# Performance work log

Hardware: AMD Instinct MI355X
Metric: run time of the kernel (lower is better)

Reference implementation:

```python
import jax, jax.numpy as jnp
import numpy as np

HEADS = 16
DIM_HEAD = 64
DIM = 1024
SEQ = 2048
BATCH = 1
THR_MIN = 0.01
THR_MAX = 0.9
LN_EPS = 1e-5
NEG = -jnp.finfo(jnp.float32).max


def _ln(x, gamma):
    # torch F.layer_norm over last dim, beta fixed to zeros
    mu = jnp.mean(x, axis=-1, keepdims=True)
    var = jnp.mean(jnp.square(x - mu), axis=-1, keepdims=True)
    return (x - mu) * jax.lax.rsqrt(var + LN_EPS) * gamma


def setup_inputs() -> dict:
    key = jax.random.key(0)
    ks = jax.random.split(key, 8)
    s = 0.02  # realistic init scale for weights
    return {
        "x": jax.random.normal(ks[0], (BATCH, SEQ, DIM), jnp.float32),
        "gamma_norm": jnp.ones((DIM,), jnp.float32),
        "Wq": jax.random.normal(ks[1], (DIM, HEADS * DIM_HEAD), jnp.float32) * s,
        "Wk": jax.random.normal(ks[2], (DIM, HEADS * DIM_HEAD), jnp.float32) * s,
        "Wv": jax.random.normal(ks[3], (DIM, HEADS * DIM_HEAD), jnp.float32) * s,
        "Wout": jax.random.normal(ks[4], (HEADS * DIM_HEAD, DIM), jnp.float32) * s,
        "gamma_out": jnp.ones((DIM,), jnp.float32),
        "W_gcn0": jax.random.normal(ks[5], (DIM_HEAD, DIM_HEAD), jnp.float32) * s,
        "b_gcn0": jnp.zeros((DIM_HEAD,), jnp.float32),
        "W_gcn1": jax.random.normal(ks[6], (DIM_HEAD, DIM_HEAD), jnp.float32) * s,
        "b_gcn1": jnp.zeros((DIM_HEAD,), jnp.float32),
        "W_lin": jax.random.normal(ks[7], (DIM_HEAD, DIM_HEAD), jnp.float32) * s,
        "b_lin": jnp.zeros((DIM_HEAD,), jnp.float32),
    }


def reference(x, gamma_norm, Wq, Wk, Wv, Wout, gamma_out,
              W_gcn0, b_gcn0, W_gcn1, b_gcn1, W_lin, b_lin):
    b, n, _ = x.shape
    h, d = HEADS, DIM_HEAD
    scale = d ** -0.5

    xn = _ln(x, gamma_norm)
    # projections, split heads: b n (h d) -> b h n d
    q = (xn @ Wq).reshape(b, n, h, d).transpose(0, 2, 1, 3) * scale
    k = (xn @ Wk).reshape(b, n, h, d).transpose(0, 2, 1, 3)
    v = (xn @ Wv).reshape(b, n, h, d).transpose(0, 2, 1, 3)

    sim = jnp.einsum("bhid,bhjd->bhij", q, k)
    causal_mask = jnp.triu(jnp.ones((n, n), bool), 1)
    sim = jnp.where(causal_mask, NEG, sim)
    attn = jax.nn.softmax(sim.astype(jnp.float32), axis=-1)  # [b,h,n,n]

    out = jnp.einsum("bhij,bhjd->bhid", attn, v)

    # --- attention-derived adjacency GCN path ---
    adj = attn.reshape(b * h, n, n) + jnp.eye(n, dtype=attn.dtype)
    adj = jnp.clip(adj, 0.0, 1.0)
    adj = jnp.where(adj < THR_MIN, 0.0, adj)
    adj = jnp.where(adj > THR_MAX, 1.0, adj)

    g = v.reshape(b * h, n, d)
    deg = jnp.sum(adj, axis=-1, keepdims=True)  # [bh, n, 1]
    # GCN layer 0 (skip connection, exact GELU like nn.GELU())
    g = jax.nn.gelu(jnp.matmul(adj, g @ W_gcn0 + b_gcn0) / deg + g, approximate=False)
    # GCN layer 1
    g = jax.nn.gelu(jnp.matmul(adj, g @ W_gcn1 + b_gcn1) / deg + g, approximate=False)
    # final linear (dropout inactive in eval)
    g = g @ W_lin + b_lin

    out = out + g.reshape(b, h, n, d)

    # merge heads: b h n d -> b n (h d), output projection + LayerNorm
    out = out.transpose(0, 2, 1, 3).reshape(b, n, h * d)
    out = _ln(out @ Wout, gamma_out)
    return out
```

## Files before the change

kernel.cpp:

```cpp
#include <hip/hip_runtime.h>
#include <hip/hip_bf16.h>
#include <math.h>
#include <stdint.h>

#define DEV __device__ __forceinline__

typedef unsigned short u16;
typedef __attribute__((ext_vector_type(8))) short s16x8;
typedef __attribute__((ext_vector_type(4))) float f32x4;
typedef __attribute__((ext_vector_type(16))) float f32x16;
typedef __attribute__((ext_vector_type(4))) unsigned u32x4;

static constexpr int SEQ = 2048;
static constexpr int DIM = 1024;
static constexpr int HEADS = 16;
static constexpr int QKVLD = 3072;
static constexpr int TOT32 = 2080;

DEV u16 f2bf(float f) {
  unsigned u = __float_as_uint(f);
  u = u + 0x7FFFu + ((u >> 16) & 1u);
  return (u16)(u >> 16);
}
DEV float bf2f(u16 b) { return __uint_as_float(((unsigned)b) << 16); }
DEV float gelu_exact(float x) { return 0.5f * x * (1.0f + erff(x * 0.70710678118654752f)); }

DEV unsigned pkbf(float lo, float hi) {
  __hip_bfloat162 h = __float22bfloat162_rn(make_float2(lo, hi));
  unsigned r; __builtin_memcpy(&r, &h, 4); return r;
}

#define MFMA16(a, b, c) __builtin_amdgcn_mfma_f32_16x16x32_bf16(a, b, c, 0, 0, 0)
#define MFMA32(a, b, c) __builtin_amdgcn_mfma_f32_32x32x16_bf16(a, b, c, 0, 0, 0)

DEV s16x8 u4_to_s8(u32x4 u) { union { u32x4 a; s16x8 b; } c; c.a = u; return c.b; }

DEV void build_frags(const float* p, int hi, s16x8* fr) {
  unsigned pw[4][2];
#pragma unroll
  for (int rq = 0; rq < 4; ++rq) {
    pw[rq][0] = pkbf(p[4 * rq + 0], p[4 * rq + 1]);
    pw[rq][1] = pkbf(p[4 * rq + 2], p[4 * rq + 3]);
  }
#pragma unroll
  for (int m = 0; m < 2; ++m) {
    unsigned x0 = __shfl_xor(pw[2 * m + 1][0], 32);
    unsigned x1 = __shfl_xor(pw[2 * m + 1][1], 32);
    unsigned y0 = __shfl_xor(pw[2 * m][0], 32);
    unsigned y1 = __shfl_xor(pw[2 * m][1], 32);
    u32x4 u;
    u[0] = hi ? x0 : pw[2 * m][0];
    u[1] = hi ? x1 : pw[2 * m][1];
    u[2] = hi ? pw[2 * m + 1][0] : y0;
    u[3] = hi ? pw[2 * m + 1][1] : y1;
    fr[m] = u4_to_s8(u);
  }
}

template<bool OUT_BF16>
__global__ __launch_bounds__(256) void ln_rows(const float* __restrict__ in,
                                               const float* __restrict__ gamma,
                                               void* __restrict__ outp) {
  int row = blockIdx.x;
  const float* x = in + (size_t)row * DIM;
  float v[4];
  float s = 0.f;
#pragma unroll
  for (int e = 0; e < 4; ++e) { v[e] = x[threadIdx.x + 256 * e]; s += v[e]; }
  __shared__ float red[8];
  int lane = threadIdx.x & 63, wid = threadIdx.x >> 6;
#pragma unroll
  for (int off = 32; off; off >>= 1) s += __shfl_xor(s, off);
  if (lane == 0) red[wid] = s;
  __syncthreads();
  float mean = (red[0] + red[1] + red[2] + red[3]) * (1.0f / DIM);
  float vs = 0.f;
#pragma unroll
  for (int e = 0; e < 4; ++e) { float d = v[e] - mean; vs += d * d; }
#pragma unroll
  for (int off = 32; off; off >>= 1) vs += __shfl_xor(vs, off);
  __syncthreads();
  if (lane == 0) red[wid] = vs;
  __syncthreads();
  float var = (red[0] + red[1] + red[2] + red[3]) * (1.0f / DIM);
  float rstd = rsqrtf(var + 1e-5f);
#pragma unroll
  for (int e = 0; e < 4; ++e) {
    int c = threadIdx.x + 256 * e;
    float o = (v[e] - mean) * rstd * gamma[c];
    if (OUT_BF16) ((u16*)outp)[(size_t)row * DIM + c] = f2bf(o);
    else          ((float*)outp)[(size_t)row * DIM + c] = o;
  }
}

__global__ __launch_bounds__(256) void wt_all(
    const float* __restrict__ Wq, const float* __restrict__ Wk, const float* __restrict__ Wv,
    const float* __restrict__ Wout, const float* __restrict__ Wg0,
    const float* __restrict__ Wg1, const float* __restrict__ Wlin,
    u16* __restrict__ WqkvT, u16* __restrict__ WoT,
    u16* __restrict__ Wg0T, u16* __restrict__ Wg1T, u16* __restrict__ WlinT) {
  int z = blockIdx.z;
  const float* src; u16* dst; int R, C, c0, r0;
  if (z < 4) {
    src = (z == 0) ? Wq : (z == 1) ? Wk : (z == 2) ? Wv : Wout;
    dst = (z == 0) ? WqkvT : (z == 1) ? WqkvT + (size_t)DIM * DIM
        : (z == 2) ? WqkvT + (size_t)2 * DIM * DIM : WoT;
    R = DIM; C = DIM; c0 = blockIdx.x * 64; r0 = blockIdx.y * 64;
  } else {
    if (blockIdx.x >= 3 || blockIdx.y > 0) return;
    src = (blockIdx.x == 0) ? Wg0 : (blockIdx.x == 1) ? Wg1 : Wlin;
    dst = (blockIdx.x == 0) ? Wg0T : (blockIdx.x == 1) ? Wg1T : WlinT;
    R = 64; C = 64; c0 = 0; r0 = 0;
  }
  __shared__ float tile[64][65];
  int tx = threadIdx.x & 63, ty = threadIdx.x >> 6;
  for (int rr = ty; rr < 64; rr += 4)
    tile[rr][tx] = src[(size_t)(r0 + rr) * C + c0 + tx];
  __syncthreads();
  for (int rr = ty; rr < 64; rr += 4)
    dst[(size_t)(c0 + rr) * R + r0 + tx] = f2bf(tile[tx][rr]);
}

__global__ __launch_bounds__(256) void pack_qkv(const u16* __restrict__ QKV,
                                                u16* __restrict__ Kp, u16* __restrict__ Vp) {
  int bx = blockIdx.x, h = blockIdx.y;
  int tid = threadIdx.x, wid = tid >> 6, lane = tid & 63;
  int l31 = lane & 31, hi = lane >> 5;
  if (bx < 64) {
    int jb = bx, fi = wid;
    s16x8 v = *(const s16x8*)(QKV + (size_t)(jb * 32 + l31) * QKVLD + 1024 + h * 64 + fi * 16 + hi * 8);
    *(s16x8*)(Kp + ((size_t)(h * 64 + jb) * 4 + fi) * 512 + lane * 8) = v;
  } else {
    int jb16 = bx - 64;
    __shared__ u16 t[16][72];
    if (tid < 128) {
      int r = tid >> 3, c = (tid & 7) * 8;
      *(s16x8*)&t[r][c] = *(const s16x8*)(QKV + (size_t)(jb16 * 16 + r) * QKVLD + 2048 + h * 64 + c);
    }
    __syncthreads();
    if (wid < 2) {
      int dh = wid;
      s16x8 v;
#pragma unroll
      for (int e = 0; e < 8; ++e) v[e] = (short)t[hi * 8 + e][dh * 32 + l31];
      *(s16x8*)(Vp + ((size_t)(h * 128 + jb16) * 2 + dh) * 512 + lane * 8) = v;
    }
  }
}

__global__ __launch_bounds__(256) void gemm_pack(
    const u16* __restrict__ Asrc, int ld, const u16* __restrict__ Wt,
    const float* __restrict__ bias, u16* __restrict__ Hp) {
  int bx = blockIdx.x, h = blockIdx.y;
  __shared__ __align__(16) u16 Ws[64][72];
  __shared__ __align__(16) u16 tt[64][72];
  int tid = threadIdx.x, lane = tid & 63, wid = tid >> 6;
  int l15 = lane & 15, lhi = lane >> 4;
  {
    int r = tid >> 2, cc = (tid & 3) * 8;
    *(s16x8*)&Ws[r][cc] = *(const s16x8*)(Wt + r * 64 + cc);
    *(s16x8*)&Ws[r][cc + 32] = *(const s16x8*)(Wt + r * 64 + cc + 32);
  }
  __syncthreads();
  int j = bx * 64 + wid * 16 + l15;
  const u16* arow = Asrc + (size_t)j * ld + h * 64;
  s16x8 a0 = *(const s16x8*)(arow + lhi * 8);
  s16x8 a1 = *(const s16x8*)(arow + 32 + lhi * 8);
  f32x4 acc[4];
#pragma unroll
  for (int c = 0; c < 4; ++c) {
    acc[c] = f32x4{0.f, 0.f, 0.f, 0.f};
    s16x8 b0 = *(const s16x8*)&Ws[c * 16 + l15][lhi * 8];
    s16x8 b1 = *(const s16x8*)&Ws[c * 16 + l15][32 + lhi * 8];
    acc[c] = MFMA16(a0, b0, acc[c]);
    acc[c] = MFMA16(a1, b1, acc[c]);
  }
  int rl = wid * 16 + lhi * 4;
#pragma unroll
  for (int c = 0; c < 4; ++c)
#pragma unroll
    for (int r = 0; r < 4; ++r)
      tt[rl + r][c * 16 + l15] = f2bf(acc[c][r] + bias[c * 16 + l15]);
  __syncthreads();
  int l31 = lane & 31, hi = lane >> 5;
#pragma unroll
  for (int dh = 0; dh < 2; ++dh) {
    s16x8 v;
#pragma unroll
    for (int e = 0; e < 8; ++e) v[e] = (short)tt[wid * 16 + hi * 8 + e][dh * 32 + l31];
    *(s16x8*)(Hp + ((size_t)(h * 128 + bx * 4 + wid) * 2 + dh) * 512 + lane * 8) = v;
  }
}

DEV void gload_lds16(const u16* g, u16* l) {
  __builtin_amdgcn_global_load_lds(
      (const __attribute__((address_space(1))) unsigned int*)g,
      (__attribute__((address_space(3))) unsigned int*)(unsigned int)(uintptr_t)l,
      16, 0, 0);
}
template<int BM, int BN, bool OUT_F32>
__global__ __launch_bounds__(256) void gemm_t(const u16* __restrict__ A,
                                              const u16* __restrict__ Bt,
                                              void* __restrict__ Cout,
                                              int Nn, int K, int Nq, float qs) {
  constexpr int MI = BM / 32;
  constexpr int NI = BN / 32;
  __shared__ __align__(16) u16 As[BM][64];
  __shared__ __align__(16) u16 Bs[BN][64];
  int tid = threadIdx.x, lane = tid & 63, wid = tid >> 6;
  int l15 = lane & 15, lhi = lane >> 4;
  int nwg = gridDim.x * gridDim.y;
  int flat = blockIdx.y * gridDim.x + blockIdx.x;
  int q8 = nwg >> 3, r8 = nwg & 7;
  int xcd = flat & 7, idx = flat >> 3;
  int wg = (xcd < r8) ? xcd * (q8 + 1) + idx : r8 * (q8 + 1) + (xcd - r8) * q8 + idx;
  int bx = wg % gridDim.x, by = wg / gridDim.x;
  int n0 = bx * BN, m0 = by * BM;
  int wr = wid >> 1, wc = wid & 1;
  float scale = (n0 < Nq) ? qs : 1.0f;
  f32x4 acc[MI][NI];
#pragma unroll
  for (int mi = 0; mi < MI; ++mi)
#pragma unroll
    for (int ni = 0; ni < NI; ++ni) acc[mi][ni] = f32x4{0.f, 0.f, 0.f, 0.f};
  int srow = lane >> 3;
  int scol = ((lane & 7) ^ srow) * 8;
  for (int k0 = 0; k0 < K; k0 += 64) {
    __syncthreads();
#pragma unroll
    for (int i = 0; i < BM / 32; ++i) {
      int row0 = (wid * (BM / 32) + i) * 8;
      gload_lds16(A + (size_t)(m0 + row0 + srow) * K + k0 + scol, &As[row0][0]);
    }
#pragma unroll
    for (int i = 0; i < BN / 32; ++i) {
      int row0 = (wid * (BN / 32) + i) * 8;
      gload_lds16(Bt + (size_t)(n0 + row0 + srow) * K + k0 + scol, &Bs[row0][0]);
    }
    __syncthreads();
#pragma unroll
    for (int ks = 0; ks < 2; ++ks) {
      s16x8 af[MI], bf[NI];
#pragma unroll
      for (int mi = 0; mi < MI; ++mi) {
        int row = wr * (BM / 2) + mi * 16 + l15;
        int c8 = (ks * 4 + lhi) ^ (row & 7);
        af[mi] = *(const s16x8*)&As[row][c8 * 8];
      }
#pragma unroll
      for (int ni = 0; ni < NI; ++ni) {
        int row = wc * (BN / 2) + ni * 16 + l15;
        int c8 = (ks * 4 + lhi) ^ (row & 7);
        bf[ni] = *(const s16x8*)&Bs[row][c8 * 8];
      }
#pragma unroll
      for (int mi = 0; mi < MI; ++mi)
#pragma unroll
        for (int ni = 0; ni < NI; ++ni)
          acc[mi][ni] = MFMA16(af[mi], bf[ni], acc[mi][ni]);
    }
  }
  int orow0 = m0 + wr * (BM / 2), ocol0 = n0 + wc * (BN / 2);
#pragma unroll
  for (int mi = 0; mi < MI; ++mi)
#pragma unroll
    for (int ni = 0; ni < NI; ++ni)
#pragma unroll
      for (int r = 0; r < 4; ++r) {
        int row = orow0 + mi * 16 + lhi * 4 + r;
        int col = ocol0 + ni * 16 + l15;
        float vv = acc[mi][ni][r] * scale;
        if (OUT_F32) ((float*)Cout)[(size_t)row * Nn + col] = vv;
        else         ((u16*)Cout)[(size_t)row * Nn + col] = f2bf(vv);
      }
}

__global__ __launch_bounds__(256) void small_gemm_add(
    const u16* __restrict__ A, int ldo, const u16* __restrict__ Wt,
    const float* __restrict__ bias, const float* __restrict__ addsrc,
    u16* __restrict__ outp) {
  __shared__ __align__(16) u16 Ws[64][72];
  int tid = threadIdx.x, lane = tid & 63, wid = tid >> 6;
  int l15 = lane & 15, lhi = lane >> 4;
  int m0 = blockIdx.x * 64;
  {
    int r = tid >> 2, cc = (tid & 3) * 8;
    *(s16x8*)&Ws[r][cc] = *(const s16x8*)(Wt + r * 64 + cc);
    *(s16x8*)&Ws[r][cc + 32] = *(const s16x8*)(Wt + r * 64 + cc + 32);
  }
  __syncthreads();
  int R = m0 + wid * 16 + l15;
  const u16* arow = A + (size_t)(R >> 4) * ldo + (R & 15) * 64;
  s16x8 a0 = *(const s16x8*)(arow + lhi * 8);
  s16x8 a1 = *(const s16x8*)(arow + 32 + lhi * 8);
  f32x4 acc[4];
#pragma unroll
  for (int c = 0; c < 4; ++c) {
    acc[c] = f32x4{0.f, 0.f, 0.f, 0.f};
    s16x8 b0 = *(const s16x8*)&Ws[c * 16 + l15][lhi * 8];
    s16x8 b1 = *(const s16x8*)&Ws[c * 16 + l15][32 + lhi * 8];
    acc[c] = MFMA16(a0, b0, acc[c]);
    acc[c] = MFMA16(a1, b1, acc[c]);
  }
  int orow = m0 + wid * 16 + lhi * 4;
#pragma unroll
  for (int c = 0; c < 4; ++c)
#pragma unroll
    for (int r = 0; r < 4; ++r) {
      int col = c * 16 + l15;
      size_t idx = (size_t)(orow + r) * 64 + col;
      outp[idx] = f2bf(acc[c][r] + bias[col] + addsrc[idx]);
    }
}

static constexpr float NEGB = -3.0e38f;
DEV int crowf(int r, int hi) { return (r & 3) + 8 * (r >> 2) + 4 * hi; }

template<bool STORE_ADJ>
__global__ __launch_bounds__(512, 4) void attn_pv(
    const u16* __restrict__ QKV, const u16* __restrict__ Kp, const u16* __restrict__ Vp,
    float* __restrict__ mbuf, float* __restrict__ lbuf, float* __restrict__ degb,
    float* __restrict__ oatt, u16* __restrict__ adjS, unsigned char* __restrict__ maskb) {
  int tid = threadIdx.x, wq = tid >> 6, lane = tid & 63;
  int l31 = lane & 31, hi = lane >> 5;
  int h = blockIdx.x & 15, sidx = blockIdx.x >> 4;
  int s = 63 - sidx;

  __shared__ float cmb[4][2][16][64];
  __shared__ float smf[8][32], slf[8][32], sdg[8][32];

  int qbase = s * 32;
  int cums = (s * (s + 1)) >> 1;
  int n = s + 1;
  int c_lo = (n * wq) >> 3, c_hi = (n * (wq + 1)) >> 3;

  s16x8 qf[4];
#pragma unroll
  for (int fi = 0; fi < 4; ++fi)
    qf[fi] = *(const s16x8*)(QKV + (size_t)(qbase + l31) * QKVLD + h * 64 + fi * 16 + hi * 8);

  float mp = NEGB, lp = 0.f;
  for (int jb = c_lo; jb < c_hi; ++jb) {
    f32x16 sa;
#pragma unroll
    for (int r = 0; r < 16; ++r) sa[r] = 0.f;
#pragma unroll
    for (int fi = 0; fi < 4; ++fi) {
      s16x8 kf = *(const s16x8*)(Kp + ((size_t)(h * 64 + jb) * 4 + fi) * 512 + lane * 8);
      sa = MFMA32(kf, qf[fi], sa);
    }
    bool diag = (jb == s);
    float vmax = NEGB;
#pragma unroll
    for (int r = 0; r < 16; ++r) {
      float v = sa[r];
      if (diag && (crowf(r, hi) > l31)) v = NEGB;
      sa[r] = v; vmax = fmaxf(vmax, v);
    }
    float mn = fmaxf(mp, vmax);
    float es = 0.f;
#pragma unroll
    for (int r = 0; r < 16; ++r) es += __expf(sa[r] - mn);
    lp = lp * __expf(mp - mn) + es;
    mp = mn;
  }
  {
    float mo = __shfl_xor(mp, 32), lo = __shfl_xor(lp, 32);
    float mn = fmaxf(mp, mo);
    lp = lp * __expf(mp - mn) + lo * __expf(mo - mn);
    mp = mn;
  }
  if (hi == 0) { smf[wq][l31] = mp; slf[wq][l31] = lp; }
  __syncthreads();
  float mt = NEGB, lt = 0.f;
#pragma unroll
  for (int w2 = 0; w2 < 8; ++w2) {
    float mo = smf[w2][l31], lo = slf[w2][l31];
    float mn = fmaxf(mt, mo);
    lt = lt * __expf(mt - mn) + lo * __expf(mo - mn);
    mt = mn;
  }
  float invl = 1.0f / lt;
  if (wq == 0 && hi == 0) {
    mbuf[(size_t)h * SEQ + qbase + l31] = mt;
    lbuf[(size_t)h * SEQ + qbase + l31] = lt;
  }

  f32x16 pv0, pv1;
#pragma unroll
  for (int r = 0; r < 16; ++r) { pv0[r] = 0.f; pv1[r] = 0.f; }
  float dacc = 0.f;
  for (int jb = c_lo; jb < c_hi; ++jb) {
    f32x16 sa;
#pragma unroll
    for (int r = 0; r < 16; ++r) sa[r] = 0.f;
#pragma unroll
    for (int fi = 0; fi < 4; ++fi) {
      s16x8 kf = *(const s16x8*)(Kp + ((size_t)(h * 64 + jb) * 4 + fi) * 512 + lane * 8);
      sa = MFMA32(kf, qf[fi], sa);
    }
    bool diag = (jb == s);
    float p[16];
#pragma unroll
    for (int r = 0; r < 16; ++r) {
      bool valid = !diag || (crowf(r, hi) <= l31);
      p[r] = valid ? __expf(sa[r] - mt) * invl : 0.f;
    }
    s16x8 pf[2]; build_frags(p, hi, pf);
#pragma unroll
    for (int m = 0; m < 2; ++m) {
      const u16* vb = Vp + ((size_t)(h * 128 + jb * 2 + m) * 2) * 512;
      pv0 = MFMA32(pf[m], *(const s16x8*)(vb + lane * 8), pv0);
      pv1 = MFMA32(pf[m], *(const s16x8*)(vb + 512 + lane * 8), pv1);
    }
    float as0 = 0.f, as1 = 0.f;
#pragma unroll
    for (int r = 0; r < 16; ++r) {
      float pp = p[r];
      float a = (diag && (crowf(r, hi) == l31)) ? 1.f
                : ((pp < 0.01f) ? 0.f : ((pp > 0.9f) ? 1.f : pp));
      p[r] = a; dacc += a;
      if (r < 8) as0 += a; else as1 += a;
    }
    unsigned flags = (__ballot(as0 > 0.f) ? 1u : 0u) | (__ballot(as1 > 0.f) ? 2u : 0u);
    if (STORE_ADJ && flags) {
      s16x8 af[2]; build_frags(p, hi, af);
      size_t fb = ((size_t)h * TOT32 + cums + jb) * 2;
#pragma unroll
      for (int m = 0; m < 2; ++m) if ((flags >> m) & 1u)
        *(s16x8*)(adjS + (fb + m) * 512 + lane * 8) = af[m];
    }
    if (lane == 0) maskb[(size_t)h * TOT32 + cums + jb] = (unsigned char)flags;
  }
  dacc += __shfl_xor(dacc, 32);
  if (hi == 0) sdg[wq][l31] = dacc;
  if (wq >= 4) {
#pragma unroll
    for (int r = 0; r < 16; ++r) {
      cmb[wq - 4][0][r][lane] = pv0[r];
      cmb[wq - 4][1][r][lane] = pv1[r];
    }
  }
  __syncthreads();
  if (wq < 4) {
#pragma unroll
    for (int r = 0; r < 16; ++r) {
      pv0[r] += cmb[wq][0][r][lane];
      pv1[r] += cmb[wq][1][r][lane];
    }
  }
  __syncthreads();
  if (wq == 2 || wq == 3) {
#pragma unroll
    for (int r = 0; r < 16; ++r) {
      cmb[wq - 2][0][r][lane] = pv0[r];
      cmb[wq - 2][1][r][lane] = pv1[r];
    }
  }
  __syncthreads();
  if (wq < 2) {
#pragma unroll
    for (int r = 0; r < 16; ++r) {
      pv0[r] += cmb[wq][0][r][lane];
      pv1[r] += cmb[wq][1][r][lane];
    }
  }
  __syncthreads();
  if (wq == 1) {
#pragma unroll
    for (int r = 0; r < 16; ++r) {
      cmb[0][0][r][lane] = pv0[r];
      cmb[0][1][r][lane] = pv1[r];
    }
  }
  __syncthreads();
  if (wq == 0) {
    if (hi == 0) {
      float dt = 0.f;
#pragma unroll
      for (int w2 = 0; w2 < 8; ++w2) dt += sdg[w2][l31];
      degb[(size_t)h * SEQ + qbase + l31] = dt;
    }
#pragma unroll
    for (int r = 0; r < 16; ++r) {
      pv0[r] += cmb[0][0][r][lane];
      pv1[r] += cmb[0][1][r][lane];
    }
#pragma unroll
    for (int r = 0; r < 16; ++r) {
      int qr = qbase + crowf(r, hi);
      oatt[(size_t)qr * DIM + h * 64 + l31] = pv0[r];
      oatt[(size_t)qr * DIM + h * 64 + 32 + l31] = pv1[r];
    }
  }
}

template<bool READ_ADJ>
__global__ __launch_bounds__(512, 4) void gcn_apply(
    const u16* __restrict__ QKV, const u16* __restrict__ Kp,
    const u16* __restrict__ Hp, const u16* __restrict__ adjS,
    const unsigned char* __restrict__ maskb,
    const float* __restrict__ mbuf, const float* __restrict__ lbuf,
    const float* __restrict__ degb,
    const u16* __restrict__ skip, int skipld, u16* __restrict__ outp) {
  int tid = threadIdx.x, wq = tid >> 6, lane = tid & 63;
  int l31 = lane & 31, hi = lane >> 5;
  int h = blockIdx.x & 15, sidx = blockIdx.x >> 4;
  int s = 63 - sidx;

  __shared__ float cmb[4][2][16][64];

  int qbase = s * 32;
  int cums = (s * (s + 1)) >> 1;
  int n = s + 1;
  int c_lo = (n * wq) >> 3, c_hi = (n * (wq + 1)) >> 3;

  f32x16 gc0, gc1;
#pragma unroll
  for (int r = 0; r < 16; ++r) { gc0[r] = 0.f; gc1[r] = 0.f; }

  if constexpr (READ_ADJ) {
    for (int jb = c_lo; jb < c_hi; ++jb) {
      unsigned flags = maskb[(size_t)h * TOT32 + cums + jb];
      if (!flags) continue;
      size_t fb = ((size_t)h * TOT32 + cums + jb) * 2;
#pragma unroll
      for (int m = 0; m < 2; ++m) if ((flags >> m) & 1u) {
        s16x8 af = *(const s16x8*)(adjS + (fb + m) * 512 + lane * 8);
        const u16* hb = Hp + ((size_t)(h * 128 + jb * 2 + m) * 2) * 512;
        gc0 = MFMA32(af, *(const s16x8*)(hb + lane * 8), gc0);
        gc1 = MFMA32(af, *(const s16x8*)(hb + 512 + lane * 8), gc1);
      }
    }
  } else {
    s16x8 qf[4];
#pragma unroll
    for (int fi = 0; fi < 4; ++fi)
      qf[fi] = *(const s16x8*)(QKV + (size_t)(qbase + l31) * QKVLD + h * 64 + fi * 16 + hi * 8);
    float mt = mbuf[(size_t)h * SEQ + qbase + l31];
    float invl = 1.0f / lbuf[(size_t)h * SEQ + qbase + l31];
    for (int jb = c_lo; jb < c_hi; ++jb) {
      unsigned flags = maskb[(size_t)h * TOT32 + cums + jb];
      if (!flags) continue;
      f32x16 sa;
#pragma unroll
      for (int r = 0; r < 16; ++r) sa[r] = 0.f;
#pragma unroll
      for (int fi = 0; fi < 4; ++fi) {
        s16x8 kf = *(const s16x8*)(Kp + ((size_t)(h * 64 + jb) * 4 + fi) * 512 + lane * 8);
        sa = MFMA32(kf, qf[fi], sa);
      }
      bool diag = (jb == s);
      float p[16];
#pragma unroll
      for (int r = 0; r < 16; ++r) {
        int cr = crowf(r, hi);
        bool valid = !diag || (cr <= l31);
        float pp = valid ? __expf(sa[r] - mt) * invl : 0.f;
        p[r] = (diag && (cr == l31)) ? 1.f
               : ((pp < 0.01f) ? 0.f : ((pp > 0.9f) ? 1.f : pp));
      }
      s16x8 af[2]; build_frags(p, hi, af);
#pragma unroll
      for (int m = 0; m < 2; ++m) if ((flags >> m) & 1u) {
        const u16* hb = Hp + ((size_t)(h * 128 + jb * 2 + m) * 2) * 512;
        gc0 = MFMA32(af[m], *(const s16x8*)(hb + lane * 8), gc0);
        gc1 = MFMA32(af[m], *(const s16x8*)(hb + 512 + lane * 8), gc1);
      }
    }
  }

  if (wq >= 4) {
#pragma unroll
    for (int r = 0; r < 16; ++r) {
      cmb[wq - 4][0][r][lane] = gc0[r];
      cmb[wq - 4][1][r][lane] = gc1[r];
    }
  }
  __syncthreads();
  if (wq < 4) {
#pragma unroll
    for (int r = 0; r < 16; ++r) {
      gc0[r] += cmb[wq][0][r][lane];
      gc1[r] += cmb[wq][1][r][lane];
    }
  }
  __syncthreads();
  if (wq == 2 || wq == 3) {
#pragma unroll
    for (int r = 0; r < 16; ++r) {
      cmb[wq - 2][0][r][lane] = gc0[r];
      cmb[wq - 2][1][r][lane] = gc1[r];
    }
  }
  __syncthreads();
  if (wq < 2) {
#pragma unroll
    for (int r = 0; r < 16; ++r) {
      gc0[r] += cmb[wq][0][r][lane];
      gc1[r] += cmb[wq][1][r][lane];
    }
  }
  __syncthreads();
  if (wq == 1) {
#pragma unroll
    for (int r = 0; r < 16; ++r) {
      cmb[0][0][r][lane] = gc0[r];
      cmb[0][1][r][lane] = gc1[r];
    }
  }
  __syncthreads();
  if (wq == 0) {
#pragma unroll
    for (int r = 0; r < 16; ++r) {
      gc0[r] += cmb[0][0][r][lane];
      gc1[r] += cmb[0][1][r][lane];
    }
#pragma unroll
    for (int r = 0; r < 16; ++r) {
      int qr = qbase + crowf(r, hi);
      float dinv = 1.0f / degb[(size_t)h * SEQ + qr];
      float sk0 = bf2f(skip[(size_t)qr * skipld + h * 64 + l31]);
      float sk1 = bf2f(skip[(size_t)qr * skipld + h * 64 + 32 + l31]);
      outp[(size_t)qr * DIM + h * 64 + l31] = f2bf(gelu_exact(gc0[r] * dinv + sk0));
      outp[(size_t)qr * DIM + h * 64 + 32 + l31] = f2bf(gelu_exact(gc1[r] * dinv + sk1));
    }
  }
}

extern "C" void kernel_launch(void* const* d_in, const int* in_sizes, int n_in,
                              void* d_out, int out_size, void* d_ws, size_t ws_size,
                              hipStream_t stream) {
  (void)in_sizes; (void)n_in; (void)out_size;
  const float* x       = (const float*)d_in[0];
  const float* gamma_n = (const float*)d_in[1];
  const float* Wq      = (const float*)d_in[2];
  const float* Wk      = (const float*)d_in[3];
  const float* Wv      = (const float*)d_in[4];
  const float* Wout    = (const float*)d_in[5];
  const float* gamma_o = (const float*)d_in[6];
  const float* Wg0     = (const float*)d_in[7];
  const float* bg0     = (const float*)d_in[8];
  const float* Wg1     = (const float*)d_in[9];
  const float* bg1     = (const float*)d_in[10];
  const float* Wlin    = (const float*)d_in[11];
  const float* blin    = (const float*)d_in[12];
  float* out = (float*)d_out;

  char* w = (char*)d_ws;
  size_t off = 0;
  auto alloc = [&](size_t bytes) -> void* {
    void* p = w + off;
    off = (off + bytes + 255) & ~(size_t)255;
    return p;
  };
  u16* xn      = (u16*)alloc((size_t)SEQ * DIM * 2);
  u16* WqkvT   = (u16*)alloc((size_t)3 * DIM * DIM * 2);
  u16* WoT     = (u16*)alloc((size_t)DIM * DIM * 2);
  u16* Wg0T    = (u16*)alloc(64 * 64 * 2);
  u16* Wg1T    = (u16*)alloc(64 * 64 * 2);
  u16* WlinT   = (u16*)alloc(64 * 64 * 2);
  u16* QKV     = (u16*)alloc((size_t)SEQ * QKVLD * 2);
  float* mbuf  = (float*)alloc((size_t)HEADS * SEQ * 4);
  float* lbuf  = (float*)alloc((size_t)HEADS * SEQ * 4);
  float* degb  = (float*)alloc((size_t)HEADS * SEQ * 4);
  float* oatt  = (float*)alloc((size_t)SEQ * DIM * 4);
  u16* g1      = (u16*)alloc((size_t)SEQ * DIM * 2);
  u16* g2      = (u16*)alloc((size_t)SEQ * DIM * 2);
  u16* Kp      = (u16*)alloc((size_t)HEADS * 64 * 4 * 512 * 2);
  u16* Vp      = (u16*)alloc((size_t)HEADS * 128 * 2 * 512 * 2);
  u16* H0p     = (u16*)alloc((size_t)HEADS * 128 * 2 * 512 * 2);
  u16* H1p     = (u16*)alloc((size_t)HEADS * 128 * 2 * 512 * 2);
  u16* Om      = (u16*)alloc((size_t)SEQ * DIM * 2);
  unsigned char* maskb = (unsigned char*)alloc((size_t)HEADS * TOT32);
  float* Y     = (float*)QKV;

  size_t adj_bytes = (size_t)HEADS * TOT32 * 2 * 512 * 2;
  bool use_adj = (off + adj_bytes) <= ws_size;
  u16* adjS = use_adj ? (u16*)alloc(adj_bytes) : nullptr;

  ln_rows<true><<<SEQ, 256, 0, stream>>>(x, gamma_n, xn);
  wt_all<<<dim3(16, 16, 5), 256, 0, stream>>>(Wq, Wk, Wv, Wout, Wg0, Wg1, Wlin,
                                              WqkvT, WoT, Wg0T, Wg1T, WlinT);
  gemm_t<64, 128, false><<<dim3(24, 32), 256, 0, stream>>>(xn, WqkvT, QKV, QKVLD, DIM,
                                                           1024, 0.125f);
  pack_qkv<<<dim3(192, 16), 256, 0, stream>>>(QKV, Kp, Vp);
  gemm_pack<<<dim3(32, 16), 256, 0, stream>>>(QKV + 2048, QKVLD, Wg0T, bg0, H0p);
  if (use_adj)
    attn_pv<true><<<1024, 512, 0, stream>>>(QKV, Kp, Vp, mbuf, lbuf, degb, oatt, adjS, maskb);
  else
    attn_pv<false><<<1024, 512, 0, stream>>>(QKV, Kp, Vp, mbuf, lbuf, degb, oatt, nullptr, maskb);
  if (use_adj)
    gcn_apply<true><<<1024, 512, 0, stream>>>(QKV, Kp, H0p, adjS, maskb, mbuf, lbuf, degb,
                                              QKV + 2048, QKVLD, g1);
  else
    gcn_apply<false><<<1024, 512, 0, stream>>>(QKV, Kp, H0p, nullptr, maskb, mbuf, lbuf, degb,
                                               QKV + 2048, QKVLD, g1);
  gemm_pack<<<dim3(32, 16), 256, 0, stream>>>(g1, DIM, Wg1T, bg1, H1p);
  if (use_adj)
    gcn_apply<true><<<1024, 512, 0, stream>>>(QKV, Kp, H1p, adjS, maskb, mbuf, lbuf, degb,
                                              g1, DIM, g2);
  else
    gcn_apply<false><<<1024, 512, 0, stream>>>(QKV, Kp, H1p, nullptr, maskb, mbuf, lbuf, degb,
                                               g1, DIM, g2);
  small_gemm_add<<<512, 256, 0, stream>>>(g2, DIM, WlinT, blin, oatt, Om);
  gemm_t<64, 64, true><<<dim3(16, 32), 256, 0, stream>>>(Om, WoT, Y, DIM, DIM, 0, 1.0f);
  ln_rows<false><<<SEQ, 256, 0, stream>>>(Y, gamma_o, out);
}
```

Baseline: 138.3 us.

## Merge prep kernels into fused launches and tree-reduce softmax statistics

Merges the input LayerNorm and the weight transposes into one kernel, and merges K/V packing with the first GCN projection into a second kernel, which removes two kernel launches and their inter-kernel gaps. Also rewrites the per-row max/sum loops in the attention stats and the adjacency passes as tree reductions, shortening the serial dependency chains. Merged grids mix heterogeneous block types with a larger shared-memory footprint per block, and the tree sums slightly change floating-point summation order.

```diff
diff --git a/kernel.cpp b/kernel.cpp
--- a/kernel.cpp
+++ b/kernel.cpp
@@ -34,6 +34,23 @@
 #define MFMA32(a, b, c) __builtin_amdgcn_mfma_f32_32x32x16_bf16(a, b, c, 0, 0, 0)
 
 DEV s16x8 u4_to_s8(u32x4 u) { union { u32x4 a; s16x8 b; } c; c.a = u; return c.b; }
+
+DEV float tsum16(const float* v) {
+  float a0 = v[0] + v[1], a1 = v[2] + v[3], a2 = v[4] + v[5], a3 = v[6] + v[7];
+  float a4 = v[8] + v[9], a5 = v[10] + v[11], a6 = v[12] + v[13], a7 = v[14] + v[15];
+  float b0 = a0 + a1, b1 = a2 + a3, b2 = a4 + a5, b3 = a6 + a7;
+  return (b0 + b1) + (b2 + b3);
+}
+DEV float tsum8(const float* v) {
+  float a0 = v[0] + v[1], a1 = v[2] + v[3], a2 = v[4] + v[5], a3 = v[6] + v[7];
+  return (a0 + a1) + (a2 + a3);
+}
+DEV float tmax16(const float* v) {
+  float a0 = fmaxf(v[0], v[1]), a1 = fmaxf(v[2], v[3]), a2 = fmaxf(v[4], v[5]), a3 = fmaxf(v[6], v[7]);
+  float a4 = fmaxf(v[8], v[9]), a5 = fmaxf(v[10], v[11]), a6 = fmaxf(v[12], v[13]), a7 = fmaxf(v[14], v[15]);
+  float b0 = fmaxf(a0, a1), b1 = fmaxf(a2, a3), b2 = fmaxf(a4, a5), b3 = fmaxf(a6, a7);
+  return fmaxf(fmaxf(b0, b1), fmaxf(b2, b3));
+}
 
 DEV void build_frags(const float* p, int hi, s16x8* fr) {
   unsigned pw[4][2];
@@ -57,10 +74,9 @@
   }
 }
 
-template<bool OUT_BF16>
-__global__ __launch_bounds__(256) void ln_rows(const float* __restrict__ in,
-                                               const float* __restrict__ gamma,
-                                               void* __restrict__ outp) {
+__global__ __launch_bounds__(256) void ln_rows_f32(const float* __restrict__ in,
+                                                   const float* __restrict__ gamma,
+                                                   float* __restrict__ outp) {
   int row = blockIdx.x;
   const float* x = in + (size_t)row * DIM;
   float v[4];
@@ -87,32 +103,64 @@
 #pragma unroll
   for (int e = 0; e < 4; ++e) {
     int c = threadIdx.x + 256 * e;
-    float o = (v[e] - mean) * rstd * gamma[c];
-    if (OUT_BF16) ((u16*)outp)[(size_t)row * DIM + c] = f2bf(o);
-    else          ((float*)outp)[(size_t)row * DIM + c] = o;
-  }
-}
-
-__global__ __launch_bounds__(256) void wt_all(
+    outp[(size_t)row * DIM + c] = (v[e] - mean) * rstd * gamma[c];
+  }
+}
+
+__global__ __launch_bounds__(256) void prep1(
+    const float* __restrict__ x, const float* __restrict__ gamma_n, u16* __restrict__ xn,
     const float* __restrict__ Wq, const float* __restrict__ Wk, const float* __restrict__ Wv,
     const float* __restrict__ Wout, const float* __restrict__ Wg0,
     const float* __restrict__ Wg1, const float* __restrict__ Wlin,
     u16* __restrict__ WqkvT, u16* __restrict__ WoT,
     u16* __restrict__ Wg0T, u16* __restrict__ Wg1T, u16* __restrict__ WlinT) {
-  int z = blockIdx.z;
+  int bid = blockIdx.x;
+  __shared__ float tile[64][65];
+  __shared__ float red[8];
+  if (bid < 2048) {
+    int row = bid;
+    const float* xr = x + (size_t)row * DIM;
+    float v[4];
+    float s = 0.f;
+#pragma unroll
+    for (int e = 0; e < 4; ++e) { v[e] = xr[threadIdx.x + 256 * e]; s += v[e]; }
+    int lane = threadIdx.x & 63, wid = threadIdx.x >> 6;
+#pragma unroll
+    for (int off = 32; off; off >>= 1) s += __shfl_xor(s, off);
+    if (lane == 0) red[wid] = s;
+    __syncthreads();
+    float mean = (red[0] + red[1] + red[2] + red[3]) * (1.0f / DIM);
+    float vs = 0.f;
+#pragma unroll
+    for (int e = 0; e < 4; ++e) { float d = v[e] - mean; vs += d * d; }
+#pragma unroll
+    for (int off = 32; off; off >>= 1) vs += __shfl_xor(vs, off);
+    __syncthreads();
+    if (lane == 0) red[wid] = vs;
+    __syncthreads();
+    float var = (red[0] + red[1] + red[2] + red[3]) * (1.0f / DIM);
+    float rstd = rsqrtf(var + 1e-5f);
+#pragma unroll
+    for (int e = 0; e < 4; ++e) {
+      int c = threadIdx.x + 256 * e;
+      xn[(size_t)row * DIM + c] = f2bf((v[e] - mean) * rstd * gamma_n[c]);
+    }
+    return;
+  }
+  int wb = bid - 2048;
   const float* src; u16* dst; int R, C, c0, r0;
-  if (z < 4) {
+  if (wb < 1024) {
+    int z = wb >> 8, rem = wb & 255;
     src = (z == 0) ? Wq : (z == 1) ? Wk : (z == 2) ? Wv : Wout;
     dst = (z == 0) ? WqkvT : (z == 1) ? WqkvT + (size_t)DIM * DIM
         : (z == 2) ? WqkvT + (size_t)2 * DIM * DIM : WoT;
-    R = DIM; C = DIM; c0 = blockIdx.x * 64; r0 = blockIdx.y * 64;
+    R = DIM; C = DIM; c0 = (rem & 15) * 64; r0 = (rem >> 4) * 64;
   } else {
-    if (blockIdx.x >= 3 || blockIdx.y > 0) return;
-    src = (blockIdx.x == 0) ? Wg0 : (blockIdx.x == 1) ? Wg1 : Wlin;
-    dst = (blockIdx.x == 0) ? Wg0T : (blockIdx.x == 1) ? Wg1T : WlinT;
+    int k = wb - 1024;
+    src = (k == 0) ? Wg0 : (k == 1) ? Wg1 : Wlin;
+    dst = (k == 0) ? Wg0T : (k == 1) ? Wg1T : WlinT;
     R = 64; C = 64; c0 = 0; r0 = 0;
   }
-  __shared__ float tile[64][65];
   int tx = threadIdx.x & 63, ty = threadIdx.x >> 6;
   for (int rr = ty; rr < 64; rr += 4)
     tile[rr][tx] = src[(size_t)(r0 + rr) * C + c0 + tx];
@@ -121,30 +169,74 @@
     dst[(size_t)(c0 + rr) * R + r0 + tx] = f2bf(tile[tx][rr]);
 }
 
-__global__ __launch_bounds__(256) void pack_qkv(const u16* __restrict__ QKV,
-                                                u16* __restrict__ Kp, u16* __restrict__ Vp) {
-  int bx = blockIdx.x, h = blockIdx.y;
+__global__ __launch_bounds__(256) void prep2(
+    const u16* __restrict__ QKV, u16* __restrict__ Kp, u16* __restrict__ Vp,
+    const u16* __restrict__ Wg0T, const float* __restrict__ bg0, u16* __restrict__ H0p) {
+  int bid = blockIdx.x;
   int tid = threadIdx.x, wid = tid >> 6, lane = tid & 63;
+  __shared__ u16 t[16][72];
+  __shared__ __align__(16) u16 Ws[64][72];
+  __shared__ __align__(16) u16 tt[64][72];
+  if (bid < 3072) {
+    int bx = bid >> 4, h = bid & 15;
+    int l31 = lane & 31, hi = lane >> 5;
+    if (bx < 64) {
+      int jb = bx, fi = wid;
+      s16x8 v = *(const s16x8*)(QKV + (size_t)(jb * 32 + l31) * QKVLD + 1024 + h * 64 + fi * 16 + hi * 8);
+      *(s16x8*)(Kp + ((size_t)(h * 64 + jb) * 4 + fi) * 512 + lane * 8) = v;
+    } else {
+      int jb16 = bx - 64;
+      if (tid < 128) {
+        int r = tid >> 3, c = (tid & 7) * 8;
+        *(s16x8*)&t[r][c] = *(const s16x8*)(QKV + (size_t)(jb16 * 16 + r) * QKVLD + 2048 + h * 64 + c);
+      }
+      __syncthreads();
+      if (wid < 2) {
+        int dh = wid;
+        s16x8 v;
+#pragma unroll
+        for (int e = 0; e < 8; ++e) v[e] = (short)t[hi * 8 + e][dh * 32 + l31];
+        *(s16x8*)(Vp + ((size_t)(h * 128 + jb16) * 2 + dh) * 512 + lane * 8) = v;
+      }
+    }
+    return;
+  }
+  int tb = bid - 3072;
+  int bx = tb >> 4, h = tb & 15;
+  int l15 = lane & 15, lhi = lane >> 4;
+  {
+    int r = tid >> 2, cc = (tid & 3) * 8;
+    *(s16x8*)&Ws[r][cc] = *(const s16x8*)(Wg0T + r * 64 + cc);
+    *(s16x8*)&Ws[r][cc + 32] = *(const s16x8*)(Wg0T + r * 64 + cc + 32);
+  }
+  __syncthreads();
+  int j = bx * 64 + wid * 16 + l15;
+  const u16* arow = QKV + (size_t)j * QKVLD + 2048 + h * 64;
+  s16x8 a0 = *(const s16x8*)(arow + lhi * 8);
+  s16x8 a1 = *(const s16x8*)(arow + 32 + lhi * 8);
+  f32x4 acc[4];
+#pragma unroll
+  for (int c = 0; c < 4; ++c) {
+    acc[c] = f32x4{0.f, 0.f, 0.f, 0.f};
+    s16x8 b0 = *(const s16x8*)&Ws[c * 16 + l15][lhi * 8];
+    s16x8 b1 = *(const s16x8*)&Ws[c * 16 + l15][32 + lhi * 8];
+    acc[c] = MFMA16(a0, b0, acc[c]);
+    acc[c] = MFMA16(a1, b1, acc[c]);
+  }
+  int rl = wid * 16 + lhi * 4;
+#pragma unroll
+  for (int c = 0; c < 4; ++c)
+#pragma unroll
+    for (int r = 0; r < 4; ++r)
+      tt[rl + r][c * 16 + l15] = f2bf(acc[c][r] + bg0[c * 16 + l15]);
+  __syncthreads();
   int l31 = lane & 31, hi = lane >> 5;
-  if (bx < 64) {
-    int jb = bx, fi = wid;
-    s16x8 v = *(const s16x8*)(QKV + (size_t)(jb * 32 + l31) * QKVLD + 1024 + h * 64 + fi * 16 + hi * 8);
-    *(s16x8*)(Kp + ((size_t)(h * 64 + jb) * 4 + fi) * 512 + lane * 8) = v;
-  } else {
-    int jb16 = bx - 64;
-    __shared__ u16 t[16][72];
-    if (tid < 128) {
-      int r = tid >> 3, c = (tid & 7) * 8;
-      *(s16x8*)&t[r][c] = *(const s16x8*)(QKV + (size_t)(jb16 * 16 + r) * QKVLD + 2048 + h * 64 + c);
-    }
-    __syncthreads();
-    if (wid < 2) {
-      int dh = wid;
-      s16x8 v;
-#pragma unroll
-      for (int e = 0; e < 8; ++e) v[e] = (short)t[hi * 8 + e][dh * 32 + l31];
-      *(s16x8*)(Vp + ((size_t)(h * 128 + jb16) * 2 + dh) * 512 + lane * 8) = v;
-    }
+#pragma unroll
+  for (int dh = 0; dh < 2; ++dh) {
+    s16x8 v;
+#pragma unroll
+    for (int e = 0; e < 8; ++e) v[e] = (short)tt[wid * 16 + hi * 8 + e][dh * 32 + l31];
+    *(s16x8*)(H0p + ((size_t)(h * 128 + bx * 4 + wid) * 2 + dh) * 512 + lane * 8) = v;
   }
 }
 
@@ -350,17 +442,19 @@
       sa = MFMA32(kf, qf[fi], sa);
     }
     bool diag = (jb == s);
-    float vmax = NEGB;
+    float sv[16];
 #pragma unroll
     for (int r = 0; r < 16; ++r) {
       float v = sa[r];
       if (diag && (crowf(r, hi) > l31)) v = NEGB;
-      sa[r] = v; vmax = fmaxf(vmax, v);
-    }
+      sv[r] = v;
+    }
+    float vmax = tmax16(sv);
     float mn = fmaxf(mp, vmax);
-    float es = 0.f;
-#pragma unroll
-    for (int r = 0; r < 16; ++r) es += __expf(sa[r] - mn);
+    float ev[16];
+#pragma unroll
+    for (int r = 0; r < 16; ++r) ev[r] = __expf(sv[r] - mn);
+    float es = tsum16(ev);
     lp = lp * __expf(mp - mn) + es;
     mp = mn;
   }
@@ -413,15 +507,15 @@
       pv0 = MFMA32(pf[m], *(const s16x8*)(vb + lane * 8), pv0);
       pv1 = MFMA32(pf[m], *(const s16x8*)(vb + 512 + lane * 8), pv1);
     }
-    float as0 = 0.f, as1 = 0.f;
 #pragma unroll
     for (int r = 0; r < 16; ++r) {
       float pp = p[r];
-      float a = (diag && (crowf(r, hi) == l31)) ? 1.f
-                : ((pp < 0.01f) ? 0.f : ((pp > 0.9f) ? 1.f : pp));
-      p[r] = a; dacc += a;
-      if (r < 8) as0 += a; else as1 += a;
-    }
+      p[r] = (diag && (crowf(r, hi) == l31)) ? 1.f
+             : ((pp < 0.01f) ? 0.f : ((pp > 0.9f) ? 1.f : pp));
+    }
+    float as0 = tsum8(&p[0]);
+    float as1 = tsum8(&p[8]);
+    dacc += as0 + as1;
     unsigned flags = (__ballot(as0 > 0.f) ? 1u : 0u) | (__ballot(as1 > 0.f) ? 2u : 0u);
     if (STORE_ADJ && flags) {
       s16x8 af[2]; build_frags(p, hi, af);
@@ -679,13 +773,11 @@
   bool use_adj = (off + adj_bytes) <= ws_size;
   u16* adjS = use_adj ? (u16*)alloc(adj_bytes) : nullptr;
 
-  ln_rows<true><<<SEQ, 256, 0, stream>>>(x, gamma_n, xn);
-  wt_all<<<dim3(16, 16, 5), 256, 0, stream>>>(Wq, Wk, Wv, Wout, Wg0, Wg1, Wlin,
-                                              WqkvT, WoT, Wg0T, Wg1T, WlinT);
+  prep1<<<2048 + 1024 + 3, 256, 0, stream>>>(x, gamma_n, xn, Wq, Wk, Wv, Wout, Wg0, Wg1, Wlin,
+                                             WqkvT, WoT, Wg0T, Wg1T, WlinT);
   gemm_t<64, 128, false><<<dim3(24, 32), 256, 0, stream>>>(xn, WqkvT, QKV, QKVLD, DIM,
                                                            1024, 0.125f);
-  pack_qkv<<<dim3(192, 16), 256, 0, stream>>>(QKV, Kp, Vp);
-  gemm_pack<<<dim3(32, 16), 256, 0, stream>>>(QKV + 2048, QKVLD, Wg0T, bg0, H0p);
+  prep2<<<3072 + 512, 256, 0, stream>>>(QKV, Kp, Vp, Wg0T, bg0, H0p);
   if (use_adj)
     attn_pv<true><<<1024, 512, 0, stream>>>(QKV, Kp, Vp, mbuf, lbuf, degb, oatt, adjS, maskb);
   else
@@ -705,5 +797,5 @@
                                                g1, DIM, g2);
   small_gemm_add<<<512, 256, 0, stream>>>(g2, DIM, WlinT, blin, oatt, Om);
   gemm_t<64, 64, true><<<dim3(16, 32), 256, 0, stream>>>(Om, WoT, Y, DIM, DIM, 0, 1.0f);
-  ln_rows<false><<<SEQ, 256, 0, stream>>>(Y, gamma_o, out);
-}
+  ln_rows_f32<<<SEQ, 256, 0, stream>>>(Y, gamma_o, out);
+}
```

Result: faster. 133.2 us (-3.7%).
